# Kernel tuning notes

Measured on AMD Instinct MI355X. Metric: run time of the kernel, lower is better.

Reference implementation:

```python
import jax, jax.numpy as jnp
import numpy as np

B, S, HID = 2, 2048, 2048
NH, NKV, HD = 32, 8, 64
EPS = 1e-6
SCALE = HD ** -0.5


def rms_norm(x, w, eps=EPS):
    xf = x.astype(jnp.float32)
    var = jnp.mean(xf * xf, axis=-1, keepdims=True)
    return (w * (xf * jax.lax.rsqrt(var + eps))).astype(x.dtype)


def rotate_half(x):
    x1, x2 = jnp.split(x, 2, axis=-1)
    return jnp.concatenate((-x2, x1), axis=-1)


def setup_inputs() -> dict:
    key = jax.random.key(0)
    ks = jax.random.split(key, 8)
    hidden_states = jax.random.normal(ks[0], (B, S, HID), jnp.float32)
    # realistic RoPE tables
    inv_freq = 1.0 / (500000.0 ** (np.arange(0, HD, 2, dtype=np.float32) / HD))
    pos = np.arange(S, dtype=np.float32)
    freqs = np.outer(pos, inv_freq)                      # [S, HD/2]
    emb = np.concatenate([freqs, freqs], axis=-1)        # [S, HD]
    cos = jnp.broadcast_to(jnp.asarray(np.cos(emb)), (B, S, HD))
    sin = jnp.broadcast_to(jnp.asarray(np.sin(emb)), (B, S, HD))
    std = HID ** -0.5
    Wq = jax.random.normal(ks[1], (NH * HD, HID), jnp.float32) * std
    Wk = jax.random.normal(ks[2], (NKV * HD, HID), jnp.float32) * std
    Wv = jax.random.normal(ks[3], (NKV * HD, HID), jnp.float32) * std
    Wo = jax.random.normal(ks[4], (HID, NH * HD), jnp.float32) * std
    q_norm_w = jnp.ones((HD,), jnp.float32)
    k_norm_w = jnp.ones((HD,), jnp.float32)
    return {"hidden_states": hidden_states, "cos": cos, "sin": sin,
            "Wq": Wq, "Wk": Wk, "Wv": Wv, "Wo": Wo,
            "q_norm_w": q_norm_w, "k_norm_w": k_norm_w}


def reference(hidden_states, cos, sin, Wq, Wk, Wv, Wo, q_norm_w, k_norm_w):
    b, s, _ = hidden_states.shape
    # QKV projections (nn.Linear: x @ W.T)
    q = (hidden_states @ Wq.T).reshape(b, s, NH, HD).transpose(0, 2, 1, 3)   # [B,NH,S,D]
    k = (hidden_states @ Wk.T).reshape(b, s, NKV, HD).transpose(0, 2, 1, 3)  # [B,NKV,S,D]
    v = (hidden_states @ Wv.T).reshape(b, s, NKV, HD).transpose(0, 2, 1, 3)
    # per-head QK RMSNorm (use_head_qk_norm=True)
    q = rms_norm(q, q_norm_w)
    k = rms_norm(k, k_norm_w)
    # RoPE, cos/sin broadcast over heads (unsqueeze dim 1)
    c = cos[:, None, :, :]
    sn = sin[:, None, :, :]
    q = q * c + rotate_half(q) * sn
    k = k * c + rotate_half(k) * sn
    # GQA: expand kv heads to query heads
    groups = NH // NKV
    k = jnp.repeat(k, groups, axis=1)
    v = jnp.repeat(v, groups, axis=1)
    # eager SDPA, causal, softmax in fp32
    scores = jnp.einsum('bhqd,bhkd->bhqk', q, k) * SCALE
    causal = jnp.tril(jnp.ones((s, s), bool))
    scores = jnp.where(causal, scores, jnp.finfo(jnp.float32).min)
    probs = jax.nn.softmax(scores.astype(jnp.float32), axis=-1).astype(q.dtype)
    attn = jnp.einsum('bhqk,bhkd->bhqd', probs, v)       # [B,NH,S,D]
    attn = attn.transpose(0, 2, 1, 3).reshape(b, s, NH * HD)
    return attn @ Wo.T
```

## Files before the change

kernel.cpp:

```cpp
#include <hip/hip_runtime.h>
#include <hip/hip_bf16.h>
#include <stdint.h>

typedef __bf16 bf16;
typedef __bf16 bf16x4 __attribute__((ext_vector_type(4)));
typedef __bf16 bf16x8 __attribute__((ext_vector_type(8)));
typedef float floatx4 __attribute__((ext_vector_type(4)));
typedef float floatx8 __attribute__((ext_vector_type(8)));

#define MFMA16(A, B, C) __builtin_amdgcn_mfma_f32_16x16x32_bf16(A, B, C, 0, 0, 0)

constexpr int Sc = 2048, HIDc = 2048, NHc = 32, NKVc = 8, HDc = 64;
constexpr float kScale = 0.125f;
constexpr float kMax = 9.0f;

__device__ __forceinline__ void async16(const bf16* g, bf16* l) {
  __builtin_amdgcn_global_load_lds(
      (const __attribute__((address_space(1))) void*)g,
      (__attribute__((address_space(3))) void*)l, 16, 0, 0);
}

__global__ __launch_bounds__(256)
void cvt5(const float* __restrict__ s0, bf16* __restrict__ d0, int n0,
          const float* __restrict__ s1, bf16* __restrict__ d1, int n1,
          const float* __restrict__ s2, bf16* __restrict__ d2, int n2,
          const float* __restrict__ s3, bf16* __restrict__ d3, int n3,
          const float* __restrict__ s4, bf16* __restrict__ d4, int n4)
{
  const float* s; bf16* d; int n;
  switch (blockIdx.y) {
    case 0: s = s0; d = d0; n = n0; break;
    case 1: s = s1; d = d1; n = n1; break;
    case 2: s = s2; d = d2; n = n2; break;
    case 3: s = s3; d = d3; n = n3; break;
    default: s = s4; d = d4; n = n4; break;
  }
  const size_t stride = (size_t)gridDim.x * blockDim.x * 8;
  for (size_t i = ((size_t)blockIdx.x * blockDim.x + threadIdx.x) * 8;
       i < (size_t)n; i += stride) {
    floatx8 f = *(const floatx8*)(s + i);
    bf16x8 o;
#pragma unroll
    for (int j = 0; j < 8; ++j) o[j] = (bf16)f[j];
    *(bf16x8*)(d + i) = o;
  }
}

template<int BM, int BN>
__device__ __forceinline__
void gemm8p_core(const bf16* __restrict__ A, const bf16* __restrict__ Bw,
                 int K, int m0, int n0, bf16* __restrict__ lds,
                 floatx4 (&acc)[BM / 32][4])
{
  constexpr int MR2  = BM / 64;
  constexpr int ALD  = BM / 128;
  constexpr int BLD  = BN / 128;
  constexpr int AH   = BM * 32;
  constexpr int BH   = BN * 32;
  constexpr int GATE = ALD + BLD;

  const int tid  = threadIdx.x;
  const int lane = tid & 63;
  const int w    = tid >> 6;
  const int r    = lane & 15;
  const int quad = lane >> 4;
  const int wm   = w >> 2;
  const int wn   = w & 3;
  const int NT   = K >> 6;

  const bf16* gA[ALD]; const bf16* gB[BLD];
#pragma unroll
  for (int i = 0; i < ALD; ++i) {
    const int ch = i * 512 + tid;
    const int lrow = ch >> 3, sl = (ch & 7) ^ (lrow & 7);
    gA[i] = A + (size_t)(m0 + (sl >> 2) * (BM / 2) + lrow) * K + (sl & 3) * 8;
  }
#pragma unroll
  for (int i = 0; i < BLD; ++i) {
    const int ch = i * 512 + tid;
    const int lrow = ch >> 3, sl = (ch & 7) ^ (lrow & 7);
    gB[i] = Bw + (size_t)(n0 + (sl >> 2) * (BN / 2) + lrow) * K + (sl & 3) * 8;
  }

  auto stA = [&](int kt, int s, int kk) {
    bf16* dst = lds + (s * 2 + kk) * AH + tid * 8;
#pragma unroll
    for (int i = 0; i < ALD; ++i)
      async16(gA[i] + kt * 64 + kk * 32, dst + i * 4096);
  };
  auto stB = [&](int kt, int s, int kk) {
    bf16* dst = lds + 4 * AH + (s * 2 + kk) * BH + tid * 8;
#pragma unroll
    for (int i = 0; i < BLD; ++i)
      async16(gB[i] + kt * 64 + kk * 32, dst + i * 4096);
  };

  const int aoff = r * 64 + (((wm << 2) + quad) ^ (r & 7)) * 8;
  const int boff = ((wn & 1) * 64 + r) * 64 + ((((wn >> 1) << 2) + quad) ^ (r & 7)) * 8;

  bf16x8 a[MR2], b[4];

#define LDB(S, KK) do { const bf16* _p = lds + 4 * AH + ((S) * 2 + (KK)) * BH + boff; \
  _Pragma("unroll") for (int n2 = 0; n2 < 4; ++n2) b[n2] = *(const bf16x8*)(_p + n2 * 1024); } while (0)
#define LDA(S, KK, MH) do { const bf16* _p = lds + ((S) * 2 + (KK)) * AH + aoff + (MH) * (BM * 16); \
  _Pragma("unroll") for (int m2 = 0; m2 < MR2; ++m2) a[m2] = *(const bf16x8*)(_p + m2 * 1024); } while (0)
#define MM(MH) do { __builtin_amdgcn_s_setprio(1); \
  _Pragma("unroll") for (int m2 = 0; m2 < MR2; ++m2) \
    _Pragma("unroll") for (int n2 = 0; n2 < 4; ++n2) \
      acc[(MH) * MR2 + m2][n2] = MFMA16(a[m2], b[n2], acc[(MH) * MR2 + m2][n2]); \
  __builtin_amdgcn_s_setprio(0); } while (0)
#define BAR() asm volatile("s_barrier" ::: "memory")
#define GATEW() do { if constexpr (GATE == 4) asm volatile("s_waitcnt vmcnt(4)" ::: "memory"); \
                     else                     asm volatile("s_waitcnt vmcnt(3)" ::: "memory"); } while (0)

  stA(0, 0, 0); stB(0, 0, 0); stA(0, 0, 1); stB(0, 0, 1);
  stA(1, 1, 0); stB(1, 1, 0);
  GATEW(); BAR();

  for (int t = 0; t < NT; ++t) {
    const int s = t & 1;
    LDB(s, 0); LDA(s, 0, 0);
    if (t + 1 < NT) stA(t + 1, s ^ 1, 1);
    BAR(); MM(0); BAR();
    LDA(s, 0, 1);
    if (t + 1 < NT) stB(t + 1, s ^ 1, 1);
    BAR(); MM(1); BAR();
    LDB(s, 1); LDA(s, 1, 0);
    if (t + 2 < NT) stA(t + 2, s, 0);
    BAR(); MM(0); BAR();
    LDA(s, 1, 1);
    if (t + 2 < NT) stB(t + 2, s, 0);
    BAR(); MM(1);
    GATEW(); BAR();
  }

#undef LDB
#undef LDA
#undef MM
#undef BAR
#undef GATEW
}

template<int MT, bool CF32>
__device__ __forceinline__
void epi_plain(const floatx4 (&acc)[MT][4], void* C, int N, int m0, int n0,
               int BMh, int wm, int wn, int r, int quad)
{
#pragma unroll
  for (int mt = 0; mt < MT; ++mt) {
#pragma unroll
    for (int nt = 0; nt < 4; ++nt) {
      const int row = m0 + wm * BMh + mt * 16 + quad * 4;
      const int col = n0 + wn * 64 + nt * 16 + r;
#pragma unroll
      for (int g = 0; g < 4; ++g) {
        const size_t ci = (size_t)(row + g) * N + col;
        if constexpr (CF32) ((float*)C)[ci] = acc[mt][nt][g];
        else                ((bf16*)C)[ci]  = (bf16)acc[mt][nt][g];
      }
    }
  }
}

template<int MT>
__device__ __forceinline__
void epi_k(const floatx4 (&acc)[MT][4], bf16* kws, const float* kw,
           const float* cp, const float* sp, int m0, int n0,
           int wm, int wn, int r, int quad)
{
  const int h = (n0 >> 6) + wn;
  const float w0 = kw[r], w1 = kw[16 + r], w2 = kw[32 + r], w3 = kw[48 + r];
#pragma unroll
  for (int mt = 0; mt < MT; ++mt) {
#pragma unroll
    for (int g = 0; g < 4; ++g) {
      const int row = m0 + wm * 128 + mt * 16 + quad * 4 + g;
      const float x0 = acc[mt][0][g], x1 = acc[mt][1][g];
      const float x2 = acc[mt][2][g], x3 = acc[mt][3][g];
      float ss = x0 * x0 + x1 * x1 + x2 * x2 + x3 * x3;
      ss += __shfl_xor(ss, 1); ss += __shfl_xor(ss, 2);
      ss += __shfl_xor(ss, 4); ss += __shfl_xor(ss, 8);
      const float rr = rsqrtf(ss * (1.0f / 64.0f) + 1e-6f);
      const float y0 = x0 * rr * w0, y1 = x1 * rr * w1;
      const float y2 = x2 * rr * w2, y3 = x3 * rr * w3;
      const float* cb = cp + (size_t)row * 64 + r;
      const float* sb = sp + (size_t)row * 64 + r;
      bf16* p = kws + (size_t)row * 512 + h * 64 + r;
      p[0]  = (bf16)(y0 * cb[0]  - y2 * sb[0]);
      p[16] = (bf16)(y1 * cb[16] - y3 * sb[16]);
      p[32] = (bf16)(y2 * cb[32] + y0 * sb[32]);
      p[48] = (bf16)(y3 * cb[48] + y1 * sb[48]);
    }
  }
}

template<int MT>
__device__ __forceinline__
void epi_v(const floatx4 (&acc)[MT][4], bf16* vt, int m0, int n0,
           int wm, int wn, int r, int quad)
{
  const int kvh = (n0 >> 6) + wn;
  const int b   = m0 >> 11;
  const int sb  = (m0 & 2047) + wm * 128 + quad * 4;
#pragma unroll
  for (int mt = 0; mt < MT; ++mt) {
#pragma unroll
    for (int nt = 0; nt < 4; ++nt) {
      const int d = nt * 16 + r;
      bf16x4 pk;
#pragma unroll
      for (int g = 0; g < 4; ++g) pk[g] = (bf16)acc[mt][nt][g];
      *(bf16x4*)(vt + ((size_t)((b * 8 + kvh) * 64 + d)) * Sc + sb + mt * 16) = pk;
    }
  }
}

__global__ __launch_bounds__(512, 2)
void qkv_gemm8(const bf16* __restrict__ hs,
               const bf16* __restrict__ Wq, const bf16* __restrict__ Wk,
               const bf16* __restrict__ Wv,
               bf16* __restrict__ q_ws, bf16* __restrict__ k_ws,
               bf16* __restrict__ vt_ws,
               const float* __restrict__ kw, const float* __restrict__ cp,
               const float* __restrict__ sp)
{
  __shared__ bf16 lds[2 * 2 * (256 + 256) * 32];
  const int wg  = blockIdx.x;
  const int swz = (wg & 7) * 24 + (wg >> 3);
  const int mi  = swz / 12, ni = swz % 12;
  const bf16* Bw; int n0;
  if (ni < 8)       { Bw = Wq; n0 = ni * 256; }
  else if (ni < 10) { Bw = Wk; n0 = (ni - 8) * 256; }
  else              { Bw = Wv; n0 = (ni - 10) * 256; }

  floatx4 acc[8][4] = {};
  gemm8p_core<256, 256>(hs, Bw, HIDc, mi * 256, n0, lds, acc);

  const int lane = threadIdx.x & 63, w = threadIdx.x >> 6;
  const int r = lane & 15, quad = lane >> 4;
  const int wm = w >> 2, wn = w & 3;
  if (ni < 8)
    epi_plain<8, false>(acc, q_ws, 2048, mi * 256, n0, 128, wm, wn, r, quad);
  else if (ni < 10)
    epi_k<8>(acc, k_ws, kw, cp, sp, mi * 256, n0, wm, wn, r, quad);
  else
    epi_v<8>(acc, vt_ws, mi * 256, n0, wm, wn, r, quad);
}

__global__ __launch_bounds__(512, 2)
void o_gemm8(const bf16* __restrict__ a_ws, const bf16* __restrict__ Wo,
             float* __restrict__ out)
{
  __shared__ bf16 lds[2 * 2 * (128 + 256) * 32];
  const int wg  = blockIdx.x;
  const int swz = (wg & 7) * 32 + (wg >> 3);
  const int mi  = swz >> 3, ni = swz & 7;

  floatx4 acc[4][4] = {};
  gemm8p_core<128, 256>(a_ws, Wo, NHc * HDc, mi * 128, ni * 256, lds, acc);

  const int lane = threadIdx.x & 63, w = threadIdx.x >> 6;
  const int r = lane & 15, quad = lane >> 4;
  const int wm = w >> 2, wn = w & 3;
  epi_plain<4, true>(acc, out, HIDc, mi * 128, ni * 256, 64, wm, wn, r, quad);
}

__global__ __launch_bounds__(256, 4)
void attn_fwd(const bf16* __restrict__ q, const bf16* __restrict__ k,
              const bf16* __restrict__ vt, bf16* __restrict__ o,
              const float* __restrict__ qw, const float* __restrict__ cp,
              const float* __restrict__ sp)
{
  __shared__ bf16 Ks[64 * 64];
  __shared__ bf16 Vs[64 * 64];
  __shared__ bf16 Ps[4][16 * 72];

  const int bi  = blockIdx.x;
  const int pa  = bi & 15;
  const int h   = (bi >> 4) & 31;
  const int b   = bi >> 9;
  const int kvh = h >> 2;
  const int tid = threadIdx.x, lane = tid & 63, w = tid >> 6;
  const int r = lane & 15, quad = lane >> 4;
  const int qt0 = 31 - pa, qt1 = pa;

  const floatx8 w0 = *(const floatx8*)(qw + quad * 8);
  const floatx8 w1 = *(const floatx8*)(qw + 32 + quad * 8);
  bf16x8 qf[2][2];
#pragma unroll
  for (int t = 0; t < 2; ++t) {
    const int qt = t == 0 ? qt0 : qt1;
    const int m = b * Sc + qt * 64 + w * 16 + r;
    const bf16* qp = q + (size_t)m * (NHc * HDc) + h * HDc + quad * 8;
    bf16x8 x0 = *(const bf16x8*)qp;
    bf16x8 x1 = *(const bf16x8*)(qp + 32);
    float ss = 0.f;
#pragma unroll
    for (int i = 0; i < 8; ++i)
      ss += (float)x0[i] * (float)x0[i] + (float)x1[i] * (float)x1[i];
    ss += __shfl_xor(ss, 16);
    ss += __shfl_xor(ss, 32);
    const float rq = rsqrtf(ss * (1.0f / 64.0f) + 1e-6f) * kScale;
    const floatx8 c0 = *(const floatx8*)(cp + (size_t)m * 64 + quad * 8);
    const floatx8 c1 = *(const floatx8*)(cp + (size_t)m * 64 + 32 + quad * 8);
    const floatx8 s0 = *(const floatx8*)(sp + (size_t)m * 64 + quad * 8);
    const floatx8 s1 = *(const floatx8*)(sp + (size_t)m * 64 + 32 + quad * 8);
    bf16x8 y0v, y1v;
#pragma unroll
    for (int i = 0; i < 8; ++i) {
      const float y0 = (float)x0[i] * rq * w0[i];
      const float y1 = (float)x1[i] * rq * w1[i];
      y0v[i] = (bf16)(y0 * c0[i] - y1 * s0[i]);
      y1v[i] = (bf16)(y1 * c1[i] + y0 * s1[i]);
    }
    qf[t][0] = y0v; qf[t][1] = y1v;
  }

  floatx4 accO[2][4] = {};
  float lsum[2][4] = {};

  const int kvr = tid >> 3;
  const int cx  = ((tid & 7) * 8) ^ (8 * (kvr & 7));
  const int xk  = 8 * (r & 7);

  const bf16* kp = k + (size_t)b * Sc * (NKVc * HDc) + kvh * HDc;
  const bf16* vp = vt + ((size_t)((b * NKVc + kvh) * 64)) * Sc;

  for (int j = 0; j <= qt0; ++j) {
    __syncthreads();
    {
      const bf16* kj = kp + (size_t)j * 64 * (NKVc * HDc);
      const bf16* vj = vp + j * 64;
      async16(kj + (size_t)kvr * (NKVc * HDc) + cx, Ks + tid * 8);
      async16(kj + (size_t)(kvr + 32) * (NKVc * HDc) + cx, Ks + (tid + 256) * 8);
      async16(vj + (size_t)kvr * Sc + cx, Vs + tid * 8);
      async16(vj + (size_t)(kvr + 32) * Sc + cx, Vs + (tid + 256) * 8);
    }
    __syncthreads();

#pragma unroll
    for (int t = 0; t < 2; ++t) {
      if (t == 1 && j > qt1) continue;
      const int qt = t == 0 ? qt0 : qt1;

      floatx4 sa[4];
#pragma unroll
      for (int nt = 0; nt < 4; ++nt) sa[nt] = floatx4{0.f, 0.f, 0.f, 0.f};
      __builtin_amdgcn_s_setprio(1);
#pragma unroll
      for (int nt = 0; nt < 4; ++nt) {
        const int kv = nt * 16 + r;
        const bf16x8 kb0 = *(const bf16x8*)(&Ks[kv * 64 + ((quad * 8) ^ xk)]);
        const bf16x8 kb1 = *(const bf16x8*)(&Ks[kv * 64 + ((quad * 8 + 32) ^ xk)]);
        sa[nt] = MFMA16(qf[t][0], kb0, sa[nt]);
        sa[nt] = MFMA16(qf[t][1], kb1, sa[nt]);
      }
      __builtin_amdgcn_s_setprio(0);

      if (j != qt) {
#pragma unroll
        for (int g = 0; g < 4; ++g)
#pragma unroll
          for (int nt = 0; nt < 4; ++nt) {
            const float p = __expf(sa[nt][g] - kMax);
            lsum[t][g] += p;
            Ps[w][(quad * 4 + g) * 72 + nt * 16 + r] = (bf16)p;
          }
      } else {
        const int maskbase = w * 16 + quad * 4;
#pragma unroll
        for (int g = 0; g < 4; ++g)
#pragma unroll
          for (int nt = 0; nt < 4; ++nt) {
            const float p = (nt * 16 + r <= maskbase + g)
                                ? __expf(sa[nt][g] - kMax) : 0.f;
            lsum[t][g] += p;
            Ps[w][(quad * 4 + g) * 72 + nt * 16 + r] = (bf16)p;
          }
      }

      const bf16x8 pa0 = *(const bf16x8*)(&Ps[w][r * 72 + quad * 8]);
      const bf16x8 pa1 = *(const bf16x8*)(&Ps[w][r * 72 + 32 + quad * 8]);
      __builtin_amdgcn_s_setprio(1);
#pragma unroll
      for (int dt = 0; dt < 4; ++dt) {
        const int d = dt * 16 + r;
        const bf16x8 vb0 = *(const bf16x8*)(&Vs[d * 64 + ((quad * 8) ^ xk)]);
        const bf16x8 vb1 = *(const bf16x8*)(&Vs[d * 64 + ((quad * 8 + 32) ^ xk)]);
        accO[t][dt] = MFMA16(pa0, vb0, accO[t][dt]);
        accO[t][dt] = MFMA16(pa1, vb1, accO[t][dt]);
      }
      __builtin_amdgcn_s_setprio(0);
    }
  }

#pragma unroll
  for (int t = 0; t < 2; ++t) {
    const int qt = t == 0 ? qt0 : qt1;
#pragma unroll
    for (int reg = 0; reg < 4; ++reg) {
      float l = lsum[t][reg];
#pragma unroll
      for (int off = 1; off < 16; off <<= 1) l += __shfl_xor(l, off);
      const float inv = 1.0f / l;
      const size_t row = (size_t)(b * Sc + qt * 64 + w * 16 + quad * 4 + reg);
#pragma unroll
      for (int dt = 0; dt < 4; ++dt)
        o[row * (NHc * HDc) + h * HDc + dt * 16 + r] = (bf16)(accO[t][dt][reg] * inv);
    }
  }
}

extern "C" void kernel_launch(void* const* d_in, const int* in_sizes, int n_in,
                              void* d_out, int out_size, void* d_ws, size_t ws_size,
                              hipStream_t stream)
{
  const float* hs = (const float*)d_in[0];
  const float* cp = (const float*)d_in[1];
  const float* sp = (const float*)d_in[2];
  const float* Wq = (const float*)d_in[3];
  const float* Wk = (const float*)d_in[4];
  const float* Wv = (const float*)d_in[5];
  const float* Wo = (const float*)d_in[6];
  const float* qw = (const float*)d_in[7];
  const float* kw = (const float*)d_in[8];
  float* out = (float*)d_out;

  char* ws = (char*)d_ws;
  bf16* q_ws  = (bf16*)ws;
  bf16* k_ws  = (bf16*)(ws + (16u << 20));
  bf16* vt_ws = (bf16*)(ws + (24u << 20));
  bf16* hs_b  = (bf16*)(ws + (28u << 20));
  bf16* Wq_b  = (bf16*)(ws + (44u << 20));
  bf16* Wk_b  = (bf16*)(ws + (52u << 20));
  bf16* Wv_b  = (bf16*)(ws + (54u << 20));
  bf16* Wo_b  = (bf16*)(ws + (56u << 20));
  bf16* a_ws  = q_ws;

  dim3 blk(256);
  cvt5<<<dim3(256, 5), blk, 0, stream>>>(
      hs, hs_b, 4096 * 2048, Wq, Wq_b, 2048 * 2048, Wk, Wk_b, 512 * 2048,
      Wv, Wv_b, 512 * 2048, Wo, Wo_b, 2048 * 2048);
  qkv_gemm8<<<dim3(192), dim3(512), 0, stream>>>(hs_b, Wq_b, Wk_b, Wv_b,
                                                 q_ws, k_ws, vt_ws, kw, cp, sp);
  attn_fwd<<<dim3(1024), blk, 0, stream>>>(q_ws, k_ws, vt_ws, a_ws, qw, cp, sp);
  o_gemm8<<<dim3(256), dim3(512), 0, stream>>>(a_ws, Wo_b, out);
}
```

Baseline: 290.6 us.

## Replace 256-wide 8-wave GEMM tiles with 128x128 4-wave tiles

Swaps the templated 8-wave GEMM core (256x256 and 128x256 tiles) for a fixed 128x128 tile core that uses 4 waves of 256 threads, with a simpler two-phase LDS pipeline per K step. The QKV grid grows from 192 to 768 blocks and the output-projection grid from 256 to 512, which aims to fill the CUs better and cut LDS use per block. In exchange each block reuses less data per load, so global/L2 traffic per FLOP goes up, and the per-phase barrier and wait scheme changes.

```diff
diff --git a/kernel.cpp b/kernel.cpp
--- a/kernel.cpp
+++ b/kernel.cpp
@@ -46,111 +46,93 @@
   }
 }
 
-template<int BM, int BN>
 __device__ __forceinline__
-void gemm8p_core(const bf16* __restrict__ A, const bf16* __restrict__ Bw,
-                 int K, int m0, int n0, bf16* __restrict__ lds,
-                 floatx4 (&acc)[BM / 32][4])
-{
-  constexpr int MR2  = BM / 64;
-  constexpr int ALD  = BM / 128;
-  constexpr int BLD  = BN / 128;
-  constexpr int AH   = BM * 32;
-  constexpr int BH   = BN * 32;
-  constexpr int GATE = ALD + BLD;
+void gemm128_core(const bf16* __restrict__ A, const bf16* __restrict__ Bw,
+                  int K, int m0, int n0, bf16* __restrict__ lds,
+                  floatx4 (&acc)[4][4])
+{
+  constexpr int IH = 128 * 32;
 
   const int tid  = threadIdx.x;
   const int lane = tid & 63;
   const int w    = tid >> 6;
   const int r    = lane & 15;
   const int quad = lane >> 4;
-  const int wm   = w >> 2;
-  const int wn   = w & 3;
+  const int wm   = w >> 1;
+  const int wn   = w & 1;
   const int NT   = K >> 6;
 
-  const bf16* gA[ALD]; const bf16* gB[BLD];
-#pragma unroll
-  for (int i = 0; i < ALD; ++i) {
-    const int ch = i * 512 + tid;
+  const bf16* gA[2]; const bf16* gB[2];
+#pragma unroll
+  for (int i = 0; i < 2; ++i) {
+    const int ch = i * 256 + tid;
     const int lrow = ch >> 3, sl = (ch & 7) ^ (lrow & 7);
-    gA[i] = A + (size_t)(m0 + (sl >> 2) * (BM / 2) + lrow) * K + (sl & 3) * 8;
-  }
-#pragma unroll
-  for (int i = 0; i < BLD; ++i) {
-    const int ch = i * 512 + tid;
-    const int lrow = ch >> 3, sl = (ch & 7) ^ (lrow & 7);
-    gB[i] = Bw + (size_t)(n0 + (sl >> 2) * (BN / 2) + lrow) * K + (sl & 3) * 8;
+    gA[i] = A  + (size_t)(m0 + (sl >> 2) * 64 + lrow) * K + (sl & 3) * 8;
+    gB[i] = Bw + (size_t)(n0 + (sl >> 2) * 64 + lrow) * K + (sl & 3) * 8;
   }
 
   auto stA = [&](int kt, int s, int kk) {
-    bf16* dst = lds + (s * 2 + kk) * AH + tid * 8;
-#pragma unroll
-    for (int i = 0; i < ALD; ++i)
-      async16(gA[i] + kt * 64 + kk * 32, dst + i * 4096);
+    bf16* dst = lds + (s * 2 + kk) * IH + tid * 8;
+#pragma unroll
+    for (int i = 0; i < 2; ++i)
+      async16(gA[i] + kt * 64 + kk * 32, dst + i * 2048);
   };
   auto stB = [&](int kt, int s, int kk) {
-    bf16* dst = lds + 4 * AH + (s * 2 + kk) * BH + tid * 8;
-#pragma unroll
-    for (int i = 0; i < BLD; ++i)
-      async16(gB[i] + kt * 64 + kk * 32, dst + i * 4096);
+    bf16* dst = lds + 4 * IH + (s * 2 + kk) * IH + tid * 8;
+#pragma unroll
+    for (int i = 0; i < 2; ++i)
+      async16(gB[i] + kt * 64 + kk * 32, dst + i * 2048);
   };
 
   const int aoff = r * 64 + (((wm << 2) + quad) ^ (r & 7)) * 8;
-  const int boff = ((wn & 1) * 64 + r) * 64 + ((((wn >> 1) << 2) + quad) ^ (r & 7)) * 8;
-
-  bf16x8 a[MR2], b[4];
-
-#define LDB(S, KK) do { const bf16* _p = lds + 4 * AH + ((S) * 2 + (KK)) * BH + boff; \
+  const int boff = r * 64 + (((wn << 2) + quad) ^ (r & 7)) * 8;
+
+  bf16x8 a[4], b[4];
+
+#define LDA(S, KK) do { const bf16* _p = lds + ((S) * 2 + (KK)) * IH + aoff; \
+  _Pragma("unroll") for (int m2 = 0; m2 < 4; ++m2) a[m2] = *(const bf16x8*)(_p + m2 * 1024); } while (0)
+#define LDB(S, KK) do { const bf16* _p = lds + 4 * IH + ((S) * 2 + (KK)) * IH + boff; \
   _Pragma("unroll") for (int n2 = 0; n2 < 4; ++n2) b[n2] = *(const bf16x8*)(_p + n2 * 1024); } while (0)
-#define LDA(S, KK, MH) do { const bf16* _p = lds + ((S) * 2 + (KK)) * AH + aoff + (MH) * (BM * 16); \
-  _Pragma("unroll") for (int m2 = 0; m2 < MR2; ++m2) a[m2] = *(const bf16x8*)(_p + m2 * 1024); } while (0)
-#define MM(MH) do { __builtin_amdgcn_s_setprio(1); \
-  _Pragma("unroll") for (int m2 = 0; m2 < MR2; ++m2) \
+#define MM() do { __builtin_amdgcn_s_setprio(1); \
+  _Pragma("unroll") for (int m2 = 0; m2 < 4; ++m2) \
     _Pragma("unroll") for (int n2 = 0; n2 < 4; ++n2) \
-      acc[(MH) * MR2 + m2][n2] = MFMA16(a[m2], b[n2], acc[(MH) * MR2 + m2][n2]); \
+      acc[m2][n2] = MFMA16(a[m2], b[n2], acc[m2][n2]); \
   __builtin_amdgcn_s_setprio(0); } while (0)
 #define BAR() asm volatile("s_barrier" ::: "memory")
-#define GATEW() do { if constexpr (GATE == 4) asm volatile("s_waitcnt vmcnt(4)" ::: "memory"); \
-                     else                     asm volatile("s_waitcnt vmcnt(3)" ::: "memory"); } while (0)
 
   stA(0, 0, 0); stB(0, 0, 0); stA(0, 0, 1); stB(0, 0, 1);
   stA(1, 1, 0); stB(1, 1, 0);
-  GATEW(); BAR();
+  asm volatile("s_waitcnt vmcnt(4)" ::: "memory"); BAR();
 
   for (int t = 0; t < NT; ++t) {
     const int s = t & 1;
-    LDB(s, 0); LDA(s, 0, 0);
-    if (t + 1 < NT) stA(t + 1, s ^ 1, 1);
-    BAR(); MM(0); BAR();
-    LDA(s, 0, 1);
-    if (t + 1 < NT) stB(t + 1, s ^ 1, 1);
-    BAR(); MM(1); BAR();
-    LDB(s, 1); LDA(s, 1, 0);
-    if (t + 2 < NT) stA(t + 2, s, 0);
-    BAR(); MM(0); BAR();
-    LDA(s, 1, 1);
-    if (t + 2 < NT) stB(t + 2, s, 0);
-    BAR(); MM(1);
-    GATEW(); BAR();
-  }
-
+    LDA(s, 0); LDB(s, 0);
+    if (t + 1 < NT) { stA(t + 1, s ^ 1, 1); stB(t + 1, s ^ 1, 1); }
+    BAR(); MM(); BAR();
+    LDA(s, 1); LDB(s, 1);
+    if (t + 2 < NT) { stA(t + 2, s, 0); stB(t + 2, s, 0); }
+    BAR(); MM();
+    if (t + 2 < NT) asm volatile("s_waitcnt vmcnt(4)" ::: "memory");
+    else            asm volatile("s_waitcnt vmcnt(0)" ::: "memory");
+    BAR();
+  }
+
+#undef LDA
 #undef LDB
-#undef LDA
 #undef MM
 #undef BAR
-#undef GATEW
-}
-
-template<int MT, bool CF32>
+}
+
+template<bool CF32>
 __device__ __forceinline__
-void epi_plain(const floatx4 (&acc)[MT][4], void* C, int N, int m0, int n0,
-               int BMh, int wm, int wn, int r, int quad)
-{
-#pragma unroll
-  for (int mt = 0; mt < MT; ++mt) {
+void epi_plain(const floatx4 (&acc)[4][4], void* C, int N, int m0, int n0,
+               int wm, int wn, int r, int quad)
+{
+#pragma unroll
+  for (int mt = 0; mt < 4; ++mt) {
 #pragma unroll
     for (int nt = 0; nt < 4; ++nt) {
-      const int row = m0 + wm * BMh + mt * 16 + quad * 4;
+      const int row = m0 + wm * 64 + mt * 16 + quad * 4;
       const int col = n0 + wn * 64 + nt * 16 + r;
 #pragma unroll
       for (int g = 0; g < 4; ++g) {
@@ -162,19 +144,18 @@
   }
 }
 
-template<int MT>
 __device__ __forceinline__
-void epi_k(const floatx4 (&acc)[MT][4], bf16* kws, const float* kw,
+void epi_k(const floatx4 (&acc)[4][4], bf16* kws, const float* kw,
            const float* cp, const float* sp, int m0, int n0,
            int wm, int wn, int r, int quad)
 {
   const int h = (n0 >> 6) + wn;
   const float w0 = kw[r], w1 = kw[16 + r], w2 = kw[32 + r], w3 = kw[48 + r];
 #pragma unroll
-  for (int mt = 0; mt < MT; ++mt) {
+  for (int mt = 0; mt < 4; ++mt) {
 #pragma unroll
     for (int g = 0; g < 4; ++g) {
-      const int row = m0 + wm * 128 + mt * 16 + quad * 4 + g;
+      const int row = m0 + wm * 64 + mt * 16 + quad * 4 + g;
       const float x0 = acc[mt][0][g], x1 = acc[mt][1][g];
       const float x2 = acc[mt][2][g], x3 = acc[mt][3][g];
       float ss = x0 * x0 + x1 * x1 + x2 * x2 + x3 * x3;
@@ -194,16 +175,15 @@
   }
 }
 
-template<int MT>
 __device__ __forceinline__
-void epi_v(const floatx4 (&acc)[MT][4], bf16* vt, int m0, int n0,
+void epi_v(const floatx4 (&acc)[4][4], bf16* vt, int m0, int n0,
            int wm, int wn, int r, int quad)
 {
   const int kvh = (n0 >> 6) + wn;
   const int b   = m0 >> 11;
-  const int sb  = (m0 & 2047) + wm * 128 + quad * 4;
-#pragma unroll
-  for (int mt = 0; mt < MT; ++mt) {
+  const int sb  = (m0 & 2047) + wm * 64 + quad * 4;
+#pragma unroll
+  for (int mt = 0; mt < 4; ++mt) {
 #pragma unroll
     for (int nt = 0; nt < 4; ++nt) {
       const int d = nt * 16 + r;
@@ -215,7 +195,7 @@
   }
 }
 
-__global__ __launch_bounds__(512, 2)
+__global__ __launch_bounds__(256, 2)
 void qkv_gemm8(const bf16* __restrict__ hs,
                const bf16* __restrict__ Wq, const bf16* __restrict__ Wk,
                const bf16* __restrict__ Wv,
@@ -224,45 +204,45 @@
                const float* __restrict__ kw, const float* __restrict__ cp,
                const float* __restrict__ sp)
 {
-  __shared__ bf16 lds[2 * 2 * (256 + 256) * 32];
+  __shared__ bf16 lds[8 * 128 * 32];
   const int wg  = blockIdx.x;
-  const int swz = (wg & 7) * 24 + (wg >> 3);
-  const int mi  = swz / 12, ni = swz % 12;
+  const int swz = (wg & 7) * 96 + (wg >> 3);
+  const int mi  = swz / 24, ni = swz % 24;
   const bf16* Bw; int n0;
-  if (ni < 8)       { Bw = Wq; n0 = ni * 256; }
-  else if (ni < 10) { Bw = Wk; n0 = (ni - 8) * 256; }
-  else              { Bw = Wv; n0 = (ni - 10) * 256; }
-
-  floatx4 acc[8][4] = {};
-  gemm8p_core<256, 256>(hs, Bw, HIDc, mi * 256, n0, lds, acc);
+  if (ni < 16)      { Bw = Wq; n0 = ni * 128; }
+  else if (ni < 20) { Bw = Wk; n0 = (ni - 16) * 128; }
+  else              { Bw = Wv; n0 = (ni - 20) * 128; }
+
+  floatx4 acc[4][4] = {};
+  gemm128_core(hs, Bw, HIDc, mi * 128, n0, lds, acc);
 
   const int lane = threadIdx.x & 63, w = threadIdx.x >> 6;
   const int r = lane & 15, quad = lane >> 4;
-  const int wm = w >> 2, wn = w & 3;
-  if (ni < 8)
-    epi_plain<8, false>(acc, q_ws, 2048, mi * 256, n0, 128, wm, wn, r, quad);
-  else if (ni < 10)
-    epi_k<8>(acc, k_ws, kw, cp, sp, mi * 256, n0, wm, wn, r, quad);
+  const int wm = w >> 1, wn = w & 1;
+  if (ni < 16)
+    epi_plain<false>(acc, q_ws, 2048, mi * 128, n0, wm, wn, r, quad);
+  else if (ni < 20)
+    epi_k(acc, k_ws, kw, cp, sp, mi * 128, n0, wm, wn, r, quad);
   else
-    epi_v<8>(acc, vt_ws, mi * 256, n0, wm, wn, r, quad);
-}
-
-__global__ __launch_bounds__(512, 2)
+    epi_v(acc, vt_ws, mi * 128, n0, wm, wn, r, quad);
+}
+
+__global__ __launch_bounds__(256, 2)
 void o_gemm8(const bf16* __restrict__ a_ws, const bf16* __restrict__ Wo,
              float* __restrict__ out)
 {
-  __shared__ bf16 lds[2 * 2 * (128 + 256) * 32];
+  __shared__ bf16 lds[8 * 128 * 32];
   const int wg  = blockIdx.x;
-  const int swz = (wg & 7) * 32 + (wg >> 3);
-  const int mi  = swz >> 3, ni = swz & 7;
+  const int swz = (wg & 7) * 64 + (wg >> 3);
+  const int mi  = swz >> 4, ni = swz & 15;
 
   floatx4 acc[4][4] = {};
-  gemm8p_core<128, 256>(a_ws, Wo, NHc * HDc, mi * 128, ni * 256, lds, acc);
+  gemm128_core(a_ws, Wo, NHc * HDc, mi * 128, ni * 128, lds, acc);
 
   const int lane = threadIdx.x & 63, w = threadIdx.x >> 6;
   const int r = lane & 15, quad = lane >> 4;
-  const int wm = w >> 2, wn = w & 3;
-  epi_plain<4, true>(acc, out, HIDc, mi * 128, ni * 256, 64, wm, wn, r, quad);
+  const int wm = w >> 1, wn = w & 1;
+  epi_plain<true>(acc, out, HIDc, mi * 128, ni * 128, wm, wn, r, quad);
 }
 
 __global__ __launch_bounds__(256, 4)
@@ -441,8 +421,8 @@
   cvt5<<<dim3(256, 5), blk, 0, stream>>>(
       hs, hs_b, 4096 * 2048, Wq, Wq_b, 2048 * 2048, Wk, Wk_b, 512 * 2048,
       Wv, Wv_b, 512 * 2048, Wo, Wo_b, 2048 * 2048);
-  qkv_gemm8<<<dim3(192), dim3(512), 0, stream>>>(hs_b, Wq_b, Wk_b, Wv_b,
-                                                 q_ws, k_ws, vt_ws, kw, cp, sp);
+  qkv_gemm8<<<dim3(768), blk, 0, stream>>>(hs_b, Wq_b, Wk_b, Wv_b,
+                                           q_ws, k_ws, vt_ws, kw, cp, sp);
   attn_fwd<<<dim3(1024), blk, 0, stream>>>(q_ws, k_ws, vt_ws, a_ws, qw, cp, sp);
-  o_gemm8<<<dim3(256), dim3(512), 0, stream>>>(a_ws, Wo_b, out);
-}
+  o_gemm8<<<dim3(512), blk, 0, stream>>>(a_ws, Wo_b, out);
+}
```

New measurement: 299.0 us. +2.9%, slower.
